# Performance work log

Hardware: AMD Instinct MI355X
Metric: run time of the kernel (lower is better)

## Reference

```python
import jax, jax.numpy as jnp
import numpy as np

B, N, F = 512, 32, 16          # batch graphs, nodes per graph, node_obs dim (last col = entity type)
H, E, NE, L = 128, 16, 3, 2    # hidden, embedding_size, num_embeddings, embed_layer_N
MAX_EDGE_DIST = 1.0


def layer_norm(x, g, b, eps=1e-5):
    mu = jnp.mean(x, axis=-1, keepdims=True)
    var = jnp.mean((x - mu) ** 2, axis=-1, keepdims=True)
    return (x - mu) / jnp.sqrt(var + eps) * g + b


def setup_inputs() -> dict:
    key = jax.random.key(0)
    ks = jax.random.split(key, 12)
    feats = jax.random.normal(ks[0], (B, N, F - 1), jnp.float32)
    ent = jax.random.randint(ks[1], (B, N), 0, NE).astype(jnp.float32)
    node_obs = jnp.concatenate([feats, ent[..., None]], axis=-1)
    adj = jax.random.uniform(ks[2], (B, N, N), jnp.float32, 0.0, 2.0)
    adj = adj * (1.0 - jnp.eye(N, dtype=jnp.float32))  # no self distance
    agent_id = jax.random.randint(ks[3], (B, 1), 0, N)
    D0 = (F - 1) + E + 1  # node feats + entity embed + edge_attr
    s = 0.05
    return dict(
        node_obs=node_obs, adj=adj, agent_id=agent_id,
        entity_embed=jax.random.normal(ks[4], (NE, E), jnp.float32) * s,
        lin1_w=jax.random.normal(ks[5], (D0, H), jnp.float32) * s, lin1_b=jnp.zeros(H, jnp.float32),
        ln1_g=jnp.ones(H, jnp.float32), ln1_b=jnp.zeros(H, jnp.float32),
        linh_w=jax.random.normal(ks[6], (L, H, H), jnp.float32) * s, linh_b=jnp.zeros((L, H), jnp.float32),
        lnh_g=jnp.ones((L, H), jnp.float32), lnh_b=jnp.zeros((L, H), jnp.float32),
        fc2a_w=jax.random.normal(ks[7], (H, H), jnp.float32) * s, fc2a_b=jnp.zeros(H, jnp.float32),
        fc2b_w=jax.random.normal(ks[8], (H, 1), jnp.float32) * s, fc2b_b=jnp.zeros(1, jnp.float32),
        fc3_w=jax.random.normal(ks[9], (H, H), jnp.float32) * s, fc3_b=jnp.zeros(H, jnp.float32),
        ln3_g=jnp.ones(H, jnp.float32), ln3_b=jnp.zeros(H, jnp.float32),
        fc4_w=jax.random.normal(ks[10], (H, H), jnp.float32) * s, fc4_b=jnp.zeros(H, jnp.float32),
        ln4_g=jnp.ones(H, jnp.float32), ln4_b=jnp.zeros(H, jnp.float32),
    )


def reference(node_obs, adj, agent_id, entity_embed,
              lin1_w, lin1_b, ln1_g, ln1_b,
              linh_w, linh_b, lnh_g, lnh_b,
              fc2a_w, fc2a_b, fc2b_w, fc2b_b,
              fc3_w, fc3_b, ln3_g, ln3_b,
              fc4_w, fc4_b, ln4_g, ln4_b):
    # processAdj: edge (r -> c) exists where 0 < adj[r,c] < max_edge_dist, edge_attr = adj value
    mask = ((adj > 0) & (adj < MAX_EDGE_DIST)).astype(adj.dtype)      # [B,N,N] (r=source, c=target)
    e = adj * mask
    # EmbedConv.message: x_j features + entity embedding + edge_attr -> MLP
    feat_j = node_obs[..., :-1]                                       # [B,N,F-1]
    ent = node_obs[..., -1].astype(jnp.int32)                         # [B,N]
    xj = jnp.concatenate([feat_j, entity_embed[ent]], axis=-1)        # [B,N,F-1+E]
    src = jnp.broadcast_to(xj[:, :, None, :], (B, N, N, xj.shape[-1]))
    pair = jnp.concatenate([src, e[..., None]], axis=-1)              # [B,r,c,D0]
    m = layer_norm(jax.nn.relu(pair @ lin1_w + lin1_b), ln1_g, ln1_b) # [B,r,c,H]
    for l in range(linh_w.shape[0]):
        m = layer_norm(jax.nn.relu(m @ linh_w[l] + linh_b[l]), lnh_g[l], lnh_b[l])
    # scatter-add aggregation at target node c (masked sum over sources r)
    h = jnp.einsum('brc,brch->bch', mask, m)                          # [B,N,H]
    hf = h.reshape(B * N, -1)
    # attention: fc2 then softmax over ALL batched-graph nodes (dim=0, as in source)
    alpha = jax.nn.softmax(jax.nn.relu(hf @ fc2a_w + fc2a_b) @ fc2b_w + fc2b_b, axis=0)  # [B*N,1]
    v = layer_norm(jax.nn.relu(hf @ fc3_w + fc3_b), ln3_g, ln3_b)
    x = layer_norm(jax.nn.relu((alpha * v) @ fc4_w + fc4_b), ln4_g, ln4_b)
    x = x.reshape(B, N, -1)
    # graph_aggr == 'node': gather agent's node features
    out = x[jnp.arange(B), agent_id[:, 0].astype(jnp.int32)]          # [B,H]
    return out
```

## Files before the change

### kernel.cpp

```cpp
#include <hip/hip_runtime.h>
#include <hip/hip_bf16.h>


typedef __attribute__((ext_vector_type(8))) __bf16 bf16x8;
typedef __attribute__((ext_vector_type(4))) float  f32x4;
typedef __attribute__((ext_vector_type(2))) float  f32x2;

__device__ float g_bf[256];

__device__ __forceinline__ unsigned short f2bf(float f) {
  union { float f; unsigned u; } v; v.f = f;
  unsigned u = v.u;
  u += 0x7FFFu + ((u >> 16) & 1u);
  return (unsigned short)(u >> 16);
}

__device__ __forceinline__ unsigned pk2bf(float a, float b) {
  union { __hip_bfloat162 h; unsigned u; } cv;
  cv.h = __float22bfloat162_rn(make_float2(a, b));
  return cv.u;
}

__device__ __forceinline__ bf16x8 lds_frag(const unsigned short* p) {
  union { uint4 u; bf16x8 v; } x;
  x.u = *(const uint4*)p;
  return x.v;
}

__device__ __forceinline__ f32x4 mfma16(bf16x8 a, bf16x8 b, f32x4 c) {
  return __builtin_amdgcn_mfma_f32_16x16x32_bf16(a, b, c, 0, 0, 0);
}

__device__ __forceinline__ float dpp_add16(float x) {
  union { float f; int i; } a, t;
  a.f = x;
  t.i = __builtin_amdgcn_update_dpp(0, a.i, 0xB1,  0xF, 0xF, true); a.f += t.f;
  t.i = __builtin_amdgcn_update_dpp(0, a.i, 0x4E,  0xF, 0xF, true); a.f += t.f;
  t.i = __builtin_amdgcn_update_dpp(0, a.i, 0x141, 0xF, 0xF, true); a.f += t.f;
  t.i = __builtin_amdgcn_update_dpp(0, a.i, 0x140, 0xF, 0xF, true); a.f += t.f;
  return a.f;
}

__device__ __forceinline__ void gll16(const void* g, void* l) {
  __builtin_amdgcn_global_load_lds(
      (const __attribute__((address_space(1))) unsigned int*)(unsigned long long)g,
      (__attribute__((address_space(3))) unsigned int*)(unsigned int)(unsigned long long)l,
      16, 0, 0);
}

__device__ __forceinline__ void stage18432(const char* g, char* l, int tid) {
  int off = tid * 16;
  gll16(g + off,         l + off);
  gll16(g + off + 4096,  l + off + 4096);
  gll16(g + off + 8192,  l + off + 8192);
  gll16(g + off + 12288, l + off + 12288);
  if (tid < 128) gll16(g + off + 16384, l + off + 16384);
}

#define WS_HB    0
#define WS_HSEL  4194304
#define WS_SWS   4456448
#define WS_STATS 4521984
#define WS_XJB   4522240
#define WS_WT0P  5570816
#define WS_W1P   5581056
#define WS_W2P   5617920
#define WS_WT3P  5654784

#define PREP_N0 524288
#define PREP_N1 (PREP_N0 + 5120)
#define PREP_N2 (PREP_N1 + 36864)
#define PREP_N3 (PREP_N2 + 17408)
#define PREP_N4 (PREP_N3 + 256)

__global__ void k_prep(const float* __restrict__ node_obs, const float* __restrict__ ent_emb,
                       const float* __restrict__ lin1_w, const float* __restrict__ linh_w,
                       const float* __restrict__ fc2a_w,
                       const float* __restrict__ ln1_g, const float* __restrict__ ln1_b,
                       const float* __restrict__ lnh_g, const float* __restrict__ lnh_b,
                       const float* __restrict__ linh_b,
                       char* __restrict__ ws) {
  int idx = blockIdx.x * 256 + threadIdx.x;
  unsigned short* xjb  = (unsigned short*)(ws + WS_XJB);
  unsigned short* WT0p = (unsigned short*)(ws + WS_WT0P);
  unsigned short* W1p  = (unsigned short*)(ws + WS_W1P);
  unsigned short* W2p  = (unsigned short*)(ws + WS_W2P);
  unsigned short* WT3p = (unsigned short*)(ws + WS_WT3P);
  if (idx < PREP_N0) {
    int row = idx >> 5, k = idx & 31;
    float val;
    if (k < 15) val = node_obs[row * 16 + k];
    else if (k < 31) {
      int ent = (int)node_obs[row * 16 + 15];
      val = ent_emb[ent * 16 + (k - 15)];
    } else val = 0.f;
    xjb[idx] = f2bf(val);
  } else if (idx < PREP_N1) {
    int r = idx - PREP_N0;
    int n = r / 40, kk = r - n * 40;
    WT0p[n * 40 + kk] = (kk < 32) ? f2bf(lin1_w[kk * 128 + n]) : (unsigned short)0;
  } else if (idx < PREP_N2) {
    int r = idx - PREP_N1;
    int l = r / 18432; r -= l * 18432;
    int h = r / 9216;  r -= h * 9216;
    int n = r / 72;    int kk = r - n * 72;
    unsigned short v = 0;
    if (kk < 64) {
      int p  = h * 64 + kk;
      int ok = 32 * (p >> 5) + 16 * (p & 1) + ((p >> 1) & 15);
      float g = l ? lnh_g[ok] : ln1_g[ok];
      v = f2bf(g * linh_w[l * 16384 + ok * 128 + n]);
    }
    (l ? W2p : W1p)[h * 9216 + n * 72 + kk] = v;
  } else if (idx < PREP_N3) {
    int r = idx - PREP_N2;
    int n = r / 136, kk = r - n * 136;
    unsigned short v = 0;
    if (kk < 128) {
      int ok = 32 * (kk >> 5) + 16 * (kk & 1) + ((kk >> 1) & 15);
      v = f2bf(fc2a_w[ok * 128 + n]);
    }
    WT3p[n * 136 + kk] = v;
  } else if (idx < PREP_N4) {
    int r = idx - PREP_N3;
    int which = r >> 7, n = r & 127;
    const float* be = which ? lnh_b : ln1_b;
    const float* w  = linh_w + which * 16384 + n;
    float a = linh_b[which * 128 + n];
#pragma unroll 8
    for (int k = 0; k < 128; ++k) a += be[k] * w[k * 128];
    g_bf[which * 128 + n] = a;
  }
}

__device__ __forceinline__ void bias_acc(f32x4 (&acc)[2][8],
                                         const float* __restrict__ gb, int li) {
#pragma unroll
  for (int tj = 0; tj < 8; ++tj) {
    float b = gb[tj * 16 + li];
#pragma unroll
    for (int ti = 0; ti < 2; ++ti)
#pragma unroll
      for (int q = 0; q < 4; ++q) acc[ti][tj][q] = b;
  }
}

__device__ __forceinline__ void epilogue_store(f32x4 (&acc)[2][8],
    unsigned short* Xs, int wv, int li, int quad) {
  const f32x2 z2 = {0.f, 0.f};
#pragma unroll
  for (int ti = 0; ti < 2; ++ti) {
#pragma unroll
    for (int rp = 0; rp < 2; ++rp) {
      f32x2 vv[8], s1 = {0.f, 0.f}, s2 = {0.f, 0.f};
#pragma unroll
      for (int tj = 0; tj < 8; ++tj) {
        f32x2 x = { acc[ti][tj][2 * rp], acc[ti][tj][2 * rp + 1] };
        x = __builtin_elementwise_max(x, z2);
        vv[tj] = x; s1 += x; s2 += x * x;
      }
      f32x2 S1 = { dpp_add16(s1.x), dpp_add16(s1.y) };
      f32x2 S2 = { dpp_add16(s2.x), dpp_add16(s2.y) };
      f32x2 mean = S1 * 0.0078125f;
      f32x2 var  = S2 * 0.0078125f - mean * mean;
      f32x2 inv  = { rsqrtf(var.x + 1e-5f), rsqrtf(var.y + 1e-5f) };
      f32x2 c0   = -mean * inv;
      int r0 = 32 * wv + ti * 16 + quad * 4 + 2 * rp;
      unsigned* d0 = (unsigned*)(Xs + r0 * 136);
      unsigned* d1 = (unsigned*)(Xs + (r0 + 1) * 136);
#pragma unroll
      for (int g4 = 0; g4 < 4; ++g4) {
        f32x2 oa = vv[2 * g4]     * inv + c0;
        f32x2 ob = vv[2 * g4 + 1] * inv + c0;
        d0[g4 * 16 + li] = pk2bf(oa.x, ob.x);
        d1[g4 * 16 + li] = pk2bf(oa.y, ob.y);
      }
    }
  }
}

__device__ __forceinline__ void epilogue_agg(f32x4 (&acc)[2][8],
    const float* __restrict__ gg, const float* __restrict__ gbe,
    float mflag ,
    unsigned short* __restrict__ hb_row, float* __restrict__ hsel_row,
    int li, int quad) {
  const f32x2 z2 = {0.f, 0.f};
  f32x2 Tp[8] = {};
  f32x2 Qp = {0.f, 0.f}, NMp = {0.f, 0.f};
#pragma unroll
  for (int ti = 0; ti < 2; ++ti) {
#pragma unroll
    for (int rp = 0; rp < 2; ++rp) {
      f32x2 vv[8], s1 = {0.f, 0.f}, s2 = {0.f, 0.f};
#pragma unroll
      for (int tj = 0; tj < 8; ++tj) {
        f32x2 x = { acc[ti][tj][2 * rp], acc[ti][tj][2 * rp + 1] };
        x = __builtin_elementwise_max(x, z2);
        vv[tj] = x; s1 += x; s2 += x * x;
      }
      f32x2 S1 = { dpp_add16(s1.x), dpp_add16(s1.y) };
      f32x2 S2 = { dpp_add16(s2.x), dpp_add16(s2.y) };
      f32x2 mean = S1 * 0.0078125f;
      f32x2 var  = S2 * 0.0078125f - mean * mean;
      f32x2 inv  = { rsqrtf(var.x + 1e-5f), rsqrtf(var.y + 1e-5f) };
      int r0 = ti * 16 + quad * 4 + 2 * rp;
      f32x2 mk = { __shfl(mflag, r0), __shfl(mflag, r0 + 1) };
      f32x2 u = mk * inv;
      Qp += u * mean; NMp += mk;
#pragma unroll
      for (int tj = 0; tj < 8; ++tj) Tp[tj] += u * vv[tj];
    }
  }
  float T[8], Q = Qp.x + Qp.y, NM = NMp.x + NMp.y;
#pragma unroll
  for (int tj = 0; tj < 8; ++tj) T[tj] = Tp[tj].x + Tp[tj].y;
#pragma unroll
  for (int tj = 0; tj < 8; ++tj) {
    T[tj] += __shfl_xor(T[tj], 16);
    T[tj] += __shfl_xor(T[tj], 32);
  }
  Q  += __shfl_xor(Q, 16);  Q  += __shfl_xor(Q, 32);
  NM += __shfl_xor(NM, 16); NM += __shfl_xor(NM, 32);
  if (quad == 0) {
    float cs[8];
#pragma unroll
    for (int tj = 0; tj < 8; ++tj) {
      int col = tj * 16 + li;
      cs[tj] = gg[col] * (T[tj] - Q) + NM * gbe[col];
    }
    unsigned* hb32 = (unsigned*)hb_row;
#pragma unroll
    for (int g4 = 0; g4 < 4; ++g4)
      hb32[g4 * 16 + li] = pk2bf(cs[2 * g4], cs[2 * g4 + 1]);
    if (hsel_row) {
#pragma unroll
      for (int tj = 0; tj < 8; ++tj) hsel_row[tj * 16 + li] = cs[tj];
    }
  }
}

#define SMP_W 34816
#define SMP_TOTAL 53248

__device__ __forceinline__ void mfma_half(f32x4 (&acc)[2][8],
    const unsigned short* Xs, const unsigned short* Wh,
    int xoff, int wv, int li, int quad) {
#pragma unroll
  for (int s = 0; s < 2; ++s) {
    bf16x8 a0 = lds_frag(Xs + (32 * wv + li) * 136 + xoff + s * 32 + quad * 8);
    bf16x8 a1 = lds_frag(Xs + (32 * wv + 16 + li) * 136 + xoff + s * 32 + quad * 8);
#pragma unroll
    for (int tj = 0; tj < 8; ++tj) {
      bf16x8 bb = lds_frag(Wh + (tj * 16 + li) * 72 + s * 32 + quad * 8);
      acc[0][tj] = mfma16(a0, bb, acc[0][tj]);
      acc[1][tj] = mfma16(a1, bb, acc[1][tj]);
    }
  }
}

__global__ __launch_bounds__(256, 3)
void k_pair(const float* __restrict__ adj, const int* __restrict__ agent_id,
            const float* __restrict__ lin1_b,
            const float* __restrict__ lnh_g, const float* __restrict__ lnh_b,
            char* __restrict__ ws) {
  __shared__ alignas(16) char smem[SMP_TOTAL];
  unsigned short* Xs = (unsigned short*)smem;
  unsigned short* Wh = (unsigned short*)(smem + SMP_W);

  const unsigned short* xjb = (const unsigned short*)(ws + WS_XJB);
  const char* WT0p = ws + WS_WT0P;
  const char* W1p  = ws + WS_W1P;
  const char* W2p  = ws + WS_W2P;

  const int tid  = threadIdx.x;
  const int b    = blockIdx.x >> 3;
  const int c0   = (blockIdx.x & 7) << 2;
  const int lane = tid & 63, li = lane & 15, quad = lane >> 4, wv = tid >> 6;
  const int c    = c0 + wv;

  {
    const uint4* src = (const uint4*)xjb;
    char* tile = smem + wv * 2560;
    int r0 = lane >> 2, p0 = lane & 3;
    uint4 v0 = src[(b * 32 + r0) * 4 + p0];
    uint4 v1 = src[(b * 32 + 16 + r0) * 4 + p0];
    *(uint4*)(tile + r0 * 80 + p0 * 16) = v0;
    *(uint4*)(tile + (16 + r0) * 80 + p0 * 16) = v1;
  }
  {
    int off = tid * 16;
    gll16(WT0p + off, smem + SMP_W + off);
    gll16(WT0p + off + 4096, smem + SMP_W + off + 4096);
    if (tid < 128) gll16(WT0p + off + 8192, smem + SMP_W + off + 8192);
  }
  float mflag = 0.f;
  if (lane < 32) {
    float a = adj[(b * 32 + lane) * 32 + c];
    float e = (a > 0.f && a < 1.f) ? a : 0.f;
    mflag = (e != 0.f) ? 1.f : 0.f;
    ((unsigned short*)(smem + wv * 2560 + lane * 80))[31] = f2bf(e);
  }
  __syncthreads();

  f32x4 acc[2][8];

  bias_acc(acc, lin1_b, li);
  {
    const unsigned short* xt = (const unsigned short*)(smem + wv * 2560);
    bf16x8 a0 = lds_frag(xt + li * 40 + quad * 8);
    bf16x8 a1 = lds_frag(xt + (li + 16) * 40 + quad * 8);
#pragma unroll
    for (int tj = 0; tj < 8; ++tj) {
      bf16x8 bb = lds_frag(Wh + (tj * 16 + li) * 40 + quad * 8);
      acc[0][tj] = mfma16(a0, bb, acc[0][tj]);
      acc[1][tj] = mfma16(a1, bb, acc[1][tj]);
    }
  }
  __syncthreads();
  stage18432(W1p, smem + SMP_W, tid);
  epilogue_store(acc, Xs, wv, li, quad);
  __syncthreads();

  bias_acc(acc, g_bf, li);
  mfma_half(acc, Xs, Wh, 0, wv, li, quad);
  __syncthreads();
  stage18432(W1p + 18432, smem + SMP_W, tid);
  __syncthreads();
  mfma_half(acc, Xs, Wh, 64, wv, li, quad);
  __syncthreads();
  stage18432(W2p, smem + SMP_W, tid);
  epilogue_store(acc, Xs, wv, li, quad);
  __syncthreads();

  bias_acc(acc, g_bf + 128, li);
  mfma_half(acc, Xs, Wh, 0, wv, li, quad);
  __syncthreads();
  stage18432(W2p + 18432, smem + SMP_W, tid);
  __syncthreads();
  mfma_half(acc, Xs, Wh, 64, wv, li, quad);

  unsigned short* hb  = (unsigned short*)(ws + WS_HB) + (b * 32 + c) * 128;
  float* hsel = (c == agent_id[b]) ? ((float*)(ws + WS_HSEL) + b * 128) : nullptr;
  epilogue_agg(acc, lnh_g + 128, lnh_b + 128,
               mflag, hb, hsel, li, quad);
}

#define SC_TOTAL 70656
__global__ __launch_bounds__(256, 2)
void k_score(const char* __restrict__ ws,
             const float* __restrict__ fc2a_b, const float* __restrict__ fc2b_w,
             const float* __restrict__ fc2b_b) {
  __shared__ alignas(16) char smem[SC_TOTAL];
  unsigned short* Xs = (unsigned short*)smem;
  unsigned short* Ws = (unsigned short*)(smem + 34816);
  float* P = (float*)(smem + 69632);
  const int tid = threadIdx.x;
  const int row0 = blockIdx.x * 128;
  const uint4* hb4 = (const uint4*)(ws + WS_HB);
  const char* WT3p = ws + WS_WT3P;
  float* sws = (float*)((char*)ws + WS_SWS);

  for (int i = tid; i < 2048; i += 256) {
    int row = i >> 4, ch = i & 15;
    uint4 v = hb4[(row0 + row) * 16 + ch];
    *(uint4*)(Xs + row * 136 + ch * 8) = v;
  }
  {
    int off = tid * 16;
#pragma unroll
    for (int it = 0; it < 8; ++it) gll16(WT3p + off + it * 4096, smem + 34816 + off + it * 4096);
    if (tid < 128) gll16(WT3p + off + 32768, smem + 34816 + off + 32768);
  }
  if (tid < 128) { P[tid] = fc2a_b[tid]; P[128 + tid] = fc2b_w[tid]; }
  __syncthreads();

  const int lane = tid & 63, li = lane & 15, quad = lane >> 4, wv = tid >> 6;
  f32x4 acc[2][8];
#pragma unroll
  for (int ti = 0; ti < 2; ++ti)
#pragma unroll
    for (int tj = 0; tj < 8; ++tj)
#pragma unroll
      for (int q = 0; q < 4; ++q) acc[ti][tj][q] = 0.f;
#pragma unroll
  for (int s = 0; s < 4; ++s) {
    bf16x8 a0 = lds_frag(Xs + (32 * wv + li) * 136 + s * 32 + quad * 8);
    bf16x8 a1 = lds_frag(Xs + (32 * wv + 16 + li) * 136 + s * 32 + quad * 8);
#pragma unroll
    for (int tj = 0; tj < 8; ++tj) {
      bf16x8 bb = lds_frag(Ws + (tj * 16 + li) * 136 + s * 32 + quad * 8);
      acc[0][tj] = mfma16(a0, bb, acc[0][tj]);
      acc[1][tj] = mfma16(a1, bb, acc[1][tj]);
    }
  }
  float bs[8], w2[8];
#pragma unroll
  for (int tj = 0; tj < 8; ++tj) {
    bs[tj] = P[tj * 16 + li];
    w2[tj] = P[128 + tj * 16 + li];
  }
  float b2 = fc2b_b[0];
#pragma unroll
  for (int ti = 0; ti < 2; ++ti) {
#pragma unroll
    for (int rg = 0; rg < 4; ++rg) {
      float t = 0.f;
#pragma unroll
      for (int tj = 0; tj < 8; ++tj) {
        float x = acc[ti][tj][rg] + bs[tj];
        x = fmaxf(x, 0.f);
        t += x * w2[tj];
      }
#pragma unroll
      for (int m = 1; m < 16; m <<= 1) t += __shfl_xor(t, m);
      if (li == 0) sws[row0 + 32 * wv + ti * 16 + quad * 4 + rg] = t + b2;
    }
  }
}

__global__ __launch_bounds__(1024)
void k_stats(char* __restrict__ ws) {
  const float* sws = (const float*)(ws + WS_SWS);
  float* stats = (float*)(ws + WS_STATS);
  __shared__ float red[1024];
  const int tid = threadIdx.x;
  float m = -3.0e38f;
  for (int i = tid; i < 16384; i += 1024) m = fmaxf(m, sws[i]);
  red[tid] = m;
  __syncthreads();
  for (int st = 512; st > 0; st >>= 1) {
    if (tid < st) red[tid] = fmaxf(red[tid], red[tid + st]);
    __syncthreads();
  }
  float mx = red[0];
  __syncthreads();
  float sm = 0.f;
  for (int i = tid; i < 16384; i += 1024) sm += __expf(sws[i] - mx);
  red[tid] = sm;
  __syncthreads();
  for (int st = 512; st > 0; st >>= 1) {
    if (tid < st) red[tid] += red[tid + st];
    __syncthreads();
  }
  if (tid == 0) { stats[0] = mx; stats[1] = red[0]; }
}

__global__ __launch_bounds__(128)
void k_final(const char* __restrict__ ws, const int* __restrict__ agent_id,
             const float* __restrict__ fc3_w, const float* __restrict__ fc3_b,
             const float* __restrict__ ln3_g, const float* __restrict__ ln3_b,
             const float* __restrict__ fc4_w, const float* __restrict__ fc4_b,
             const float* __restrict__ ln4_g, const float* __restrict__ ln4_b,
             float* __restrict__ out) {
  const float* hsel  = (const float*)(ws + WS_HSEL);
  const float* sws   = (const float*)(ws + WS_SWS);
  const float* stats = (const float*)(ws + WS_STATS);
  __shared__ float xrow[128];
  __shared__ float red[8];
  const int tid = threadIdx.x;
  const int b = blockIdx.x;
  xrow[tid] = hsel[b * 128 + tid];
  __syncthreads();
  float t = fc3_b[tid];
  for (int k = 0; k < 128; ++k) t += xrow[k] * fc3_w[k * 128 + tid];
  t = fmaxf(t, 0.f);
  float s1 = t, s2 = t * t;
#pragma unroll
  for (int m = 1; m < 64; m <<= 1) { s1 += __shfl_xor(s1, m); s2 += __shfl_xor(s2, m); }
  if ((tid & 63) == 0) { red[(tid >> 6) * 2] = s1; red[(tid >> 6) * 2 + 1] = s2; }
  __syncthreads();
  s1 = red[0] + red[2]; s2 = red[1] + red[3];
  float mean = s1 * 0.0078125f;
  float var  = s2 * 0.0078125f - mean * mean;
  float inv  = rsqrtf(var + 1e-5f);
  float v = (t - mean) * inv * ln3_g[tid] + ln3_b[tid];
  float alpha = __expf(sws[b * 32 + agent_id[b]] - stats[0]) / stats[1];
  __syncthreads();
  xrow[tid] = alpha * v;
  __syncthreads();
  float x = fc4_b[tid];
  for (int k = 0; k < 128; ++k) x += xrow[k] * fc4_w[k * 128 + tid];
  x = fmaxf(x, 0.f);
  s1 = x; s2 = x * x;
#pragma unroll
  for (int m = 1; m < 64; m <<= 1) { s1 += __shfl_xor(s1, m); s2 += __shfl_xor(s2, m); }
  if ((tid & 63) == 0) { red[4 + (tid >> 6) * 2] = s1; red[5 + (tid >> 6) * 2] = s2; }
  __syncthreads();
  s1 = red[4] + red[6]; s2 = red[5] + red[7];
  mean = s1 * 0.0078125f;
  var  = s2 * 0.0078125f - mean * mean;
  inv  = rsqrtf(var + 1e-5f);
  out[b * 128 + tid] = (x - mean) * inv * ln4_g[tid] + ln4_b[tid];
}

extern "C" void kernel_launch(void* const* d_in, const int* in_sizes, int n_in,
                              void* d_out, int out_size, void* d_ws, size_t ws_size,
                              hipStream_t stream) {
  (void)in_sizes; (void)n_in; (void)out_size; (void)ws_size;
  const float* node_obs = (const float*)d_in[0];
  const float* adj      = (const float*)d_in[1];
  const int*   agent_id = (const int*)d_in[2];
  const float* ent_emb  = (const float*)d_in[3];
  const float* lin1_w   = (const float*)d_in[4];
  const float* lin1_b   = (const float*)d_in[5];
  const float* ln1_g    = (const float*)d_in[6];
  const float* ln1_beta = (const float*)d_in[7];
  const float* linh_w   = (const float*)d_in[8];
  const float* linh_b   = (const float*)d_in[9];
  const float* lnh_g    = (const float*)d_in[10];
  const float* lnh_b    = (const float*)d_in[11];
  const float* fc2a_b   = (const float*)d_in[13];
  const float* fc2b_w   = (const float*)d_in[14];
  const float* fc2b_b   = (const float*)d_in[15];
  const float* fc3_w    = (const float*)d_in[16];
  const float* fc3_b    = (const float*)d_in[17];
  const float* ln3_g    = (const float*)d_in[18];
  const float* ln3_b    = (const float*)d_in[19];
  const float* fc4_w    = (const float*)d_in[20];
  const float* fc4_b    = (const float*)d_in[21];
  const float* ln4_g    = (const float*)d_in[22];
  const float* ln4_b    = (const float*)d_in[23];
  float* out = (float*)d_out;
  char* ws = (char*)d_ws;

  k_prep<<<(PREP_N4 + 255) / 256, 256, 0, stream>>>(node_obs, ent_emb, lin1_w, linh_w,
                                                    (const float*)d_in[12],
                                                    ln1_g, ln1_beta, lnh_g, lnh_b,
                                                    linh_b, ws);
  k_pair<<<4096, 256, 0, stream>>>(adj, agent_id, lin1_b, lnh_g, lnh_b, ws);
  k_score<<<128, 256, 0, stream>>>(ws, fc2a_b, fc2b_w, fc2b_b);
  k_stats<<<1, 1024, 0, stream>>>(ws);
  k_final<<<512, 128, 0, stream>>>(ws, agent_id,
                                   fc3_w, fc3_b, ln3_g, ln3_b,
                                   fc4_w, fc4_b, ln4_g, ln4_b, out);
}
```

Before: 203.2 us.

## Compact masked edges and pack two sparse target nodes per wave

Adds a k_mask pre-pass that counts live edges (0<adj<1) per target node and sorts nodes into big and small lists with atomics. k_pair then gathers only the live source rows into the MFMA tile, so a wave handles one dense node or two sparse nodes (at most 16 edges each), and blocks beyond the task count exit early. The aim is to skip MLP work on masked-out edge pairs, which make up roughly half of all pairs. This costs an extra kernel launch, atomics, a compaction step via ballot/popc, and a scratch region reused from the WS_SWS area. Also, the order in which nodes are written becomes nondeterministic.

Result: slower. 322.4 us (+58.6%).

```diff
diff --git a/kernel.cpp b/kernel.cpp
--- a/kernel.cpp
+++ b/kernel.cpp
@@ -72,6 +72,7 @@
 #define PREP_N2 (PREP_N1 + 36864)
 #define PREP_N3 (PREP_N2 + 17408)
 #define PREP_N4 (PREP_N3 + 256)
+#define PREP_N5 (PREP_N4 + 2)
 
 __global__ void k_prep(const float* __restrict__ node_obs, const float* __restrict__ ent_emb,
                        const float* __restrict__ lin1_w, const float* __restrict__ linh_w,
@@ -130,7 +131,26 @@
 #pragma unroll 8
     for (int k = 0; k < 128; ++k) a += be[k] * w[k * 128];
     g_bf[which * 128 + n] = a;
-  }
+  } else if (idx < PREP_N5) {
+    ((unsigned*)(ws + WS_STATS + 16))[idx - PREP_N4] = 0u;
+  }
+}
+
+__global__ __launch_bounds__(256)
+void k_mask(const float* __restrict__ adj, char* __restrict__ ws) {
+  int p = blockIdx.x * 256 + threadIdx.x;
+  int b = p >> 5, c = p & 31;
+  int cnt = 0;
+#pragma unroll 8
+  for (int r = 0; r < 32; ++r) {
+    float a = adj[(b * 32 + r) * 32 + c];
+    cnt += (a > 0.f && a < 1.f) ? 1 : 0;
+  }
+  unsigned* tcnt = (unsigned*)(ws + WS_STATS + 16);
+  unsigned short* bigl = (unsigned short*)(ws + WS_SWS);
+  unsigned short* smal = bigl + 16384;
+  if (cnt > 16) { unsigned i = atomicAdd(&tcnt[0], 1u); bigl[i] = (unsigned short)p; }
+  else          { unsigned i = atomicAdd(&tcnt[1], 1u); smal[i] = (unsigned short)p; }
 }
 
 __device__ __forceinline__ void bias_acc(f32x4 (&acc)[2][8],
@@ -179,19 +199,53 @@
   }
 }
 
-__device__ __forceinline__ void epilogue_agg(f32x4 (&acc)[2][8],
+__device__ __forceinline__ void agg_reduce_write(float (&T)[8], float Q, float NM,
     const float* __restrict__ gg, const float* __restrict__ gbe,
-    float mflag ,
-    unsigned short* __restrict__ hb_row, float* __restrict__ hsel_row,
+    int pair, const int* __restrict__ agent_id, char* __restrict__ ws,
+    int li, int quad) {
+#pragma unroll
+  for (int tj = 0; tj < 8; ++tj) {
+    T[tj] += __shfl_xor(T[tj], 16);
+    T[tj] += __shfl_xor(T[tj], 32);
+  }
+  Q += __shfl_xor(Q, 16); Q += __shfl_xor(Q, 32);
+  if (quad != 0 || pair < 0) return;
+  float cs[8];
+#pragma unroll
+  for (int tj = 0; tj < 8; ++tj) {
+    int col = tj * 16 + li;
+    cs[tj] = gg[col] * (T[tj] - Q) + NM * gbe[col];
+  }
+  unsigned* hb32 = (unsigned*)((unsigned short*)(ws + WS_HB) + pair * 128);
+#pragma unroll
+  for (int g4 = 0; g4 < 4; ++g4)
+    hb32[g4 * 16 + li] = pk2bf(cs[2 * g4], cs[2 * g4 + 1]);
+  int b = pair >> 5;
+  if ((pair & 31) == agent_id[b]) {
+    float* hs = (float*)(ws + WS_HSEL) + b * 128;
+#pragma unroll
+    for (int tj = 0; tj < 8; ++tj) hs[tj * 16 + li] = cs[tj];
+  }
+}
+
+__device__ __forceinline__ void epilogue_agg2(f32x4 (&acc)[2][8],
+    const float* __restrict__ gg, const float* __restrict__ gbe,
+    int big, int cnt0, int cnt1, int p0, int p1,
+    const int* __restrict__ agent_id, char* __restrict__ ws,
     int li, int quad) {
   const f32x2 z2 = {0.f, 0.f};
-  f32x2 Tp[8] = {};
-  f32x2 Qp = {0.f, 0.f}, NMp = {0.f, 0.f};
+  float T0[8], T1[8], Q0 = 0.f, Q1 = 0.f;
 #pragma unroll
   for (int ti = 0; ti < 2; ++ti) {
+    f32x2 Tp[8];
+#pragma unroll
+    for (int tj = 0; tj < 8; ++tj) Tp[tj] = z2;
+    f32x2 Qp = z2;
+    float lim   = big ? (float)(cnt0 + cnt1) : (float)(ti ? cnt1 : cnt0);
+    float rbase = (float)((big ? ti * 16 : 0) + quad * 4);
 #pragma unroll
     for (int rp = 0; rp < 2; ++rp) {
-      f32x2 vv[8], s1 = {0.f, 0.f}, s2 = {0.f, 0.f};
+      f32x2 vv[8], s1 = z2, s2 = z2;
 #pragma unroll
       for (int tj = 0; tj < 8; ++tj) {
         f32x2 x = { acc[ti][tj][2 * rp], acc[ti][tj][2 * rp + 1] };
@@ -203,39 +257,31 @@
       f32x2 mean = S1 * 0.0078125f;
       f32x2 var  = S2 * 0.0078125f - mean * mean;
       f32x2 inv  = { rsqrtf(var.x + 1e-5f), rsqrtf(var.y + 1e-5f) };
-      int r0 = ti * 16 + quad * 4 + 2 * rp;
-      f32x2 mk = { __shfl(mflag, r0), __shfl(mflag, r0 + 1) };
+      float r0f = rbase + (float)(2 * rp);
+      f32x2 mk = { (r0f < lim) ? 1.f : 0.f, (r0f + 1.f < lim) ? 1.f : 0.f };
       f32x2 u = mk * inv;
-      Qp += u * mean; NMp += mk;
+      Qp += u * mean;
 #pragma unroll
       for (int tj = 0; tj < 8; ++tj) Tp[tj] += u * vv[tj];
     }
-  }
-  float T[8], Q = Qp.x + Qp.y, NM = NMp.x + NMp.y;
-#pragma unroll
-  for (int tj = 0; tj < 8; ++tj) T[tj] = Tp[tj].x + Tp[tj].y;
-#pragma unroll
-  for (int tj = 0; tj < 8; ++tj) {
-    T[tj] += __shfl_xor(T[tj], 16);
-    T[tj] += __shfl_xor(T[tj], 32);
-  }
-  Q  += __shfl_xor(Q, 16);  Q  += __shfl_xor(Q, 32);
-  NM += __shfl_xor(NM, 16); NM += __shfl_xor(NM, 32);
-  if (quad == 0) {
-    float cs[8];
-#pragma unroll
-    for (int tj = 0; tj < 8; ++tj) {
-      int col = tj * 16 + li;
-      cs[tj] = gg[col] * (T[tj] - Q) + NM * gbe[col];
-    }
-    unsigned* hb32 = (unsigned*)hb_row;
-#pragma unroll
-    for (int g4 = 0; g4 < 4; ++g4)
-      hb32[g4 * 16 + li] = pk2bf(cs[2 * g4], cs[2 * g4 + 1]);
-    if (hsel_row) {
-#pragma unroll
-      for (int tj = 0; tj < 8; ++tj) hsel_row[tj * 16 + li] = cs[tj];
-    }
+    if (ti == 0) {
+#pragma unroll
+      for (int tj = 0; tj < 8; ++tj) T0[tj] = Tp[tj].x + Tp[tj].y;
+      Q0 = Qp.x + Qp.y;
+    } else {
+#pragma unroll
+      for (int tj = 0; tj < 8; ++tj) T1[tj] = Tp[tj].x + Tp[tj].y;
+      Q1 = Qp.x + Qp.y;
+    }
+  }
+  if (big) {
+#pragma unroll
+    for (int tj = 0; tj < 8; ++tj) T0[tj] += T1[tj];
+    Q0 += Q1;
+    agg_reduce_write(T0, Q0, (float)(cnt0 + cnt1), gg, gbe, p0, agent_id, ws, li, quad);
+  } else {
+    agg_reduce_write(T0, Q0, (float)cnt0, gg, gbe, p0, agent_id, ws, li, quad);
+    agg_reduce_write(T1, Q1, (float)cnt1, gg, gbe, p1, agent_id, ws, li, quad);
   }
 }
 
@@ -273,19 +319,56 @@
   const char* W2p  = ws + WS_W2P;
 
   const int tid  = threadIdx.x;
-  const int b    = blockIdx.x >> 3;
-  const int c0   = (blockIdx.x & 7) << 2;
   const int lane = tid & 63, li = lane & 15, quad = lane >> 4, wv = tid >> 6;
-  const int c    = c0 + wv;
+
+  const unsigned* tcnt = (const unsigned*)(ws + WS_STATS + 16);
+  const int n_big = (int)tcnt[0], n_small = (int)tcnt[1];
+  const int n_task = n_big + ((n_small + 1) >> 1);
+  if ((int)(blockIdx.x * 4) >= n_task) return;
+  const int slot = blockIdx.x * 4 + wv;
+  const unsigned short* bigl = (const unsigned short*)(ws + WS_SWS);
+  const unsigned short* smal = bigl + 16384;
+  int p0 = -1, p1 = -1, big = 0;
+  if (slot < n_big) { p0 = bigl[slot]; big = 1; }
+  else if (slot < n_task) {
+    int j = slot - n_big;
+    p0 = smal[2 * j];
+    if (2 * j + 1 < n_small) p1 = smal[2 * j + 1];
+  }
+
+  const int r = lane & 31, hh = lane >> 5;
+  int pp = big ? (hh ? -1 : p0) : (hh ? p1 : p0);
+  float a_val = 0.f;
+  if (pp >= 0) a_val = adj[(((pp >> 5) * 32 + r) * 32) + (pp & 31)];
+  const bool live = (a_val > 0.f) && (a_val < 1.f);
+  unsigned long long bal = __ballot(live);
+  unsigned hm = hh ? (unsigned)(bal >> 32) : (unsigned)bal;
+  int pre = __popc(hm & ((1u << r) - 1u));
+  int slot_in = big ? pre : (hh * 16 + pre);
+  int cnt0, cnt1;
+  if (big) { int ca = __popc((unsigned)bal); cnt0 = ca < 16 ? ca : 16; cnt1 = ca - cnt0; }
+  else     { cnt0 = __popc((unsigned)bal); cnt1 = __popc((unsigned)(bal >> 32)); }
+  unsigned* scr = (unsigned*)(smem + 10240 + wv * 128);
+  if (live) scr[slot_in] = (unsigned)r;
 
   {
     const uint4* src = (const uint4*)xjb;
     char* tile = smem + wv * 2560;
-    int r0 = lane >> 2, p0 = lane & 3;
-    uint4 v0 = src[(b * 32 + r0) * 4 + p0];
-    uint4 v1 = src[(b * 32 + 16 + r0) * 4 + p0];
-    *(uint4*)(tile + r0 * 80 + p0 * 16) = v0;
-    *(uint4*)(tile + (16 + r0) * 80 + p0 * 16) = v1;
+    int j0 = lane >> 2, j1 = 16 + (lane >> 2), pt = lane & 3;
+    int ca = cnt0 + cnt1;
+    bool v0 = j0 < (big ? ca : cnt0);
+    bool v1 = big ? (j1 < ca) : ((j1 - 16) < cnt1);
+    int b0 = (p0 < 0 ? 0 : p0 >> 5);
+    int b1 = (p1 < 0 ? 0 : p1 >> 5);
+    int sb1 = big ? b0 : b1;
+    unsigned sr0 = v0 ? scr[j0] : 0u;
+    unsigned sr1 = v1 ? scr[j1] : 0u;
+    uint4 z4 = {0u, 0u, 0u, 0u};
+    uint4 q0 = v0 ? src[(b0 * 32 + (int)sr0) * 4 + pt] : z4;
+    uint4 q1 = v1 ? src[(sb1 * 32 + (int)sr1) * 4 + pt] : z4;
+    *(uint4*)(tile + j0 * 80 + pt * 16) = q0;
+    *(uint4*)(tile + j1 * 80 + pt * 16) = q1;
+    if (live) ((unsigned short*)(tile + slot_in * 80))[31] = f2bf(a_val);
   }
   {
     int off = tid * 16;
@@ -293,13 +376,6 @@
     gll16(WT0p + off + 4096, smem + SMP_W + off + 4096);
     if (tid < 128) gll16(WT0p + off + 8192, smem + SMP_W + off + 8192);
   }
-  float mflag = 0.f;
-  if (lane < 32) {
-    float a = adj[(b * 32 + lane) * 32 + c];
-    float e = (a > 0.f && a < 1.f) ? a : 0.f;
-    mflag = (e != 0.f) ? 1.f : 0.f;
-    ((unsigned short*)(smem + wv * 2560 + lane * 80))[31] = f2bf(e);
-  }
   __syncthreads();
 
   f32x4 acc[2][8];
@@ -339,10 +415,8 @@
   __syncthreads();
   mfma_half(acc, Xs, Wh, 64, wv, li, quad);
 
-  unsigned short* hb  = (unsigned short*)(ws + WS_HB) + (b * 32 + c) * 128;
-  float* hsel = (c == agent_id[b]) ? ((float*)(ws + WS_HSEL) + b * 128) : nullptr;
-  epilogue_agg(acc, lnh_g + 128, lnh_b + 128,
-               mflag, hb, hsel, li, quad);
+  epilogue_agg2(acc, lnh_g + 128, lnh_b + 128, big, cnt0, cnt1, p0, p1,
+                agent_id, ws, li, quad);
 }
 
 #define SC_TOTAL 70656
@@ -523,10 +597,11 @@
   float* out = (float*)d_out;
   char* ws = (char*)d_ws;
 
-  k_prep<<<(PREP_N4 + 255) / 256, 256, 0, stream>>>(node_obs, ent_emb, lin1_w, linh_w,
+  k_prep<<<(PREP_N5 + 255) / 256, 256, 0, stream>>>(node_obs, ent_emb, lin1_w, linh_w,
                                                     (const float*)d_in[12],
                                                     ln1_g, ln1_beta, lnh_g, lnh_b,
                                                     linh_b, ws);
+  k_mask<<<64, 256, 0, stream>>>(adj, ws);
   k_pair<<<4096, 256, 0, stream>>>(adj, agent_id, lin1_b, lnh_g, lnh_b, ws);
   k_score<<<128, 256, 0, stream>>>(ws, fc2a_b, fc2b_w, fc2b_b);
   k_stats<<<1, 1024, 0, stream>>>(ws);
```
